# Performance work log

Hardware: AMD Instinct MI355X
Metric: run time of the kernel (lower is better)

Reference implementation:

```python
import jax, jax.numpy as jnp
import numpy as np

B, S, H = 2, 2048, 1024
NH, HD = 16, 64
WINDOW = 1024
ROPE_THETA = 10000.0
MAX_POS = 2048


def _rope_tables(dtype=jnp.float32):
    # RotaryEmbedding cache: inv_freq over even dims, emb = cat(freqs, freqs)
    inv_freq = 1.0 / (ROPE_THETA ** (jnp.arange(0, HD, 2, dtype=jnp.float32) / HD))
    t = jnp.arange(MAX_POS, dtype=jnp.float32)
    freqs = jnp.einsum('i,j->ij', t, inv_freq)          # [MAX_POS, HD//2]
    emb = jnp.concatenate([freqs, freqs], axis=-1)      # [MAX_POS, HD]
    return jnp.cos(emb).astype(dtype), jnp.sin(emb).astype(dtype)


def _rotate_half(x):
    x1, x2 = x[..., : HD // 2], x[..., HD // 2:]
    return jnp.concatenate([-x2, x1], axis=-1)


def setup_inputs() -> dict:
    key = jax.random.key(0)
    ks = jax.random.split(key, 5)
    sc = 0.02
    hidden_states = jax.random.normal(ks[0], (B, S, H), dtype=jnp.float32)
    position_ids = jnp.tile(jnp.arange(S, dtype=jnp.int64)[None, :], (B, 1))
    wq = jax.random.normal(ks[1], (H, H), dtype=jnp.float32) * sc
    wk = jax.random.normal(ks[2], (H, H), dtype=jnp.float32) * sc
    wv = jax.random.normal(ks[3], (H, H), dtype=jnp.float32) * sc
    wo = jax.random.normal(ks[4], (H, H), dtype=jnp.float32) * sc
    zeros = jnp.zeros((H,), dtype=jnp.float32)
    return {"hidden_states": hidden_states, "position_ids": position_ids,
            "wq": wq, "bq": zeros, "wk": wk, "bk": zeros,
            "wv": wv, "bv": zeros, "wo": wo, "bo": zeros}


def reference(hidden_states, position_ids, wq, bq, wk, bk, wv, bv, wo, bo):
    b, s, _ = hidden_states.shape
    # projections (nn.Linear: x @ W.T + b), split heads -> [B, NH, S, HD]
    def proj(w, bias):
        y = hidden_states @ w.T + bias
        return y.reshape(b, s, NH, HD).transpose(0, 2, 1, 3)
    q, k, v = proj(wq, bq), proj(wk, bk), proj(wv, bv)

    # RoPE: gather cos/sin at position_ids, broadcast over heads
    cos_t, sin_t = _rope_tables(hidden_states.dtype)
    pos = jnp.clip(position_ids, 0, MAX_POS - 1)
    cos = cos_t[pos][:, None, :, :]   # [B, 1, S, HD]
    sin = sin_t[pos][:, None, :, :]
    q = q * cos + _rotate_half(q) * sin
    k = k * cos + _rotate_half(k) * sin

    # scaled dot-product attention with causal + sliding-window band mask
    scores = jnp.einsum('bhqd,bhkd->bhqk', q, k) / jnp.sqrt(jnp.asarray(HD, hidden_states.dtype))
    i = jnp.arange(s)[:, None]
    j = jnp.arange(s)[None, :]
    allowed = (j <= i) & (i - j < WINDOW)          # banded causal mask [S, S]
    neg = jnp.asarray(jnp.finfo(hidden_states.dtype).min, hidden_states.dtype)
    scores = jnp.where(allowed[None, None, :, :], scores, neg)
    probs = jax.nn.softmax(scores, axis=-1)
    ctx = jnp.einsum('bhqk,bhkd->bhqd', probs, v)  # [B, NH, S, HD]
    ctx = ctx.transpose(0, 2, 1, 3).reshape(b, s, H)
    return ctx @ wo.T + bo
```

## Files before the change

### kernel.cpp

```cpp
#include <hip/hip_runtime.h>

#define BATCH 2
#define SDIM 2048
#define HDIM 1024
#define NHEADS 16
#define HEADD 64
#define WIN 1024

typedef __bf16 bf16x8 __attribute__((ext_vector_type(8)));
typedef __bf16 bf16x4 __attribute__((ext_vector_type(4)));
typedef float f32x4 __attribute__((ext_vector_type(4)));
typedef unsigned short u16x8 __attribute__((ext_vector_type(8)));

__device__ __forceinline__ unsigned short bf16_rne(float f) {
    union { float f; unsigned u; } x; x.f = f;
    unsigned r = x.u + 0x7fffu + ((x.u >> 16) & 1u);
    return (unsigned short)(r >> 16);
}

__device__ __forceinline__ void gload_lds16(const unsigned short* g, unsigned short* l) {
    __builtin_amdgcn_global_load_lds(
        (const __attribute__((address_space(1))) void*)g,
        (__attribute__((address_space(3))) void*)l, 16, 0, 0);
}

__global__ __launch_bounds__(256) void prep_kernel(
    const float* __restrict__ hs, const float* __restrict__ wq, const float* __restrict__ wk,
    const float* __restrict__ wv, const float* __restrict__ wo,
    unsigned short* __restrict__ Xb, unsigned short* __restrict__ Wqkv,
    unsigned short* __restrict__ Wob, float2* __restrict__ cstab)
{
    int i = blockIdx.x * 256 + threadIdx.x;
    if (i < 2097152) {
        const float* src; unsigned short* dst; int off;
        if (i < 1048576)      { src = hs; dst = Xb;             off = i; }
        else if (i < 1310720) { src = wq; dst = Wqkv;           off = i - 1048576; }
        else if (i < 1572864) { src = wk; dst = Wqkv + 1048576; off = i - 1310720; }
        else if (i < 1835008) { src = wv; dst = Wqkv + 2097152; off = i - 1572864; }
        else                  { src = wo; dst = Wob;            off = i - 1835008; }
        float4 v = reinterpret_cast<const float4*>(src)[off];
        ushort4 r;
        r.x = bf16_rne(v.x); r.y = bf16_rne(v.y); r.z = bf16_rne(v.z); r.w = bf16_rne(v.w);
        reinterpret_cast<ushort4*>(dst)[off] = r;
    } else {
        int j = i - 2097152;
        int p = j >> 5, f = j & 31;
        float inv = (float)pow(10000.0, -(double)f / 32.0);
        float ang = (float)p * inv;
        cstab[j] = make_float2(cosf(ang), sinf(ang));
    }
}

__global__ __launch_bounds__(256) void vtrans_kernel(
    const unsigned short* __restrict__ in, unsigned short* __restrict__ out)
{
    __shared__ __align__(16) unsigned short T[64 * 72];
    int s0 = blockIdx.x * 64, h = blockIdx.y, b = blockIdx.z;
    long hb = (long)(b * NHEADS + h) * SDIM * HEADD;
    int t = threadIdx.x;
    int sr = t >> 2, sc = (t & 3) * 16;
    u16x8 v0 = *(const u16x8*)&in[hb + (long)(s0 + sr) * HEADD + sc];
    u16x8 v1 = *(const u16x8*)&in[hb + (long)(s0 + sr) * HEADD + sc + 8];
    #pragma unroll
    for (int j = 0; j < 8; j++) {
        T[(sc + j) * 72     + (sr ^ (sc & 48))] = (unsigned short)v0[j];
        T[(sc + 8 + j) * 72 + (sr ^ (sc & 48))] = (unsigned short)v1[j];
    }
    __syncthreads();
    int dr = t >> 2, dc = (t & 3) * 16;
    int cb = dc ^ (dr & 48);
    u16x8 o0 = *(const u16x8*)&T[dr * 72 + cb];
    u16x8 o1 = *(const u16x8*)&T[dr * 72 + cb + 8];
    *(u16x8*)&out[hb + (long)dr * SDIM + s0 + dc]     = o0;
    *(u16x8*)&out[hb + (long)dr * SDIM + s0 + dc + 8] = o1;
}

__device__ __forceinline__ void mfma_gemm_128(
    const unsigned short* __restrict__ A,
    const unsigned short* __restrict__ Bm,
    int m0, int n0, int tid,
    unsigned short* lA, unsigned short* lB,
    f32x4 acc[4][4])
{
    const int K = 1024;
    const int BUF = 128 * 32;
    int lane = tid & 63, wid = tid >> 6;
    int wm = wid >> 1, wn = wid & 1;
    int lane15 = lane & 15, lhi = lane >> 4;
    int lrow = lane >> 2;
    int swz = (lane & 3) ^ ((lane >> 3) & 3);
    const unsigned short* ga0 = A  + (long)(m0 + wid * 32      + lrow) * K + swz * 8;
    const unsigned short* ga1 = A  + (long)(m0 + wid * 32 + 16 + lrow) * K + swz * 8;
    const unsigned short* gb0 = Bm + (long)(n0 + wid * 32      + lrow) * K + swz * 8;
    const unsigned short* gb1 = Bm + (long)(n0 + wid * 32 + 16 + lrow) * K + swz * 8;
    unsigned short* la0 = lA + (wid * 32)      * 32;
    unsigned short* la1 = lA + (wid * 32 + 16) * 32;
    unsigned short* lb0 = lB + (wid * 32)      * 32;
    unsigned short* lb1 = lB + (wid * 32 + 16) * 32;
    int ru = (lhi ^ ((lane15 >> 1) & 3)) * 8;

#define STAGE_G(boff, kt) \
    gload_lds16(ga0 + (kt) * 32, la0 + (boff)); \
    gload_lds16(ga1 + (kt) * 32, la1 + (boff)); \
    gload_lds16(gb0 + (kt) * 32, lb0 + (boff)); \
    gload_lds16(gb1 + (kt) * 32, lb1 + (boff));

#define COMPUTE_G(off) { \
    bf16x8 af[4], bfr[4]; \
    _Pragma("unroll") \
    for (int f = 0; f < 4; f++) { \
        af[f]  = *(const bf16x8*)&lA[(off) + (wm * 64 + f * 16 + lane15) * 32 + ru]; \
        bfr[f] = *(const bf16x8*)&lB[(off) + (wn * 64 + f * 16 + lane15) * 32 + ru]; \
    } \
    _Pragma("unroll") \
    for (int i = 0; i < 4; i++) \
        _Pragma("unroll") \
        for (int j = 0; j < 4; j++) \
            acc[i][j] = __builtin_amdgcn_mfma_f32_16x16x32_bf16(af[i], bfr[j], acc[i][j], 0, 0, 0); \
}

#define WAITB(n) \
    asm volatile("s_waitcnt vmcnt(" #n ")" ::: "memory"); \
    __builtin_amdgcn_s_barrier(); \
    asm volatile("" ::: "memory");

    STAGE_G(0, 0);
    STAGE_G(BUF, 1);
    #pragma unroll 1
    for (int t = 0; t < 30; t += 3) {
        WAITB(4);
        STAGE_G(2 * BUF, t + 2);
        COMPUTE_G(0);
        WAITB(4);
        STAGE_G(0, t + 3);
        COMPUTE_G(BUF);
        WAITB(4);
        STAGE_G(BUF, t + 4);
        COMPUTE_G(2 * BUF);
    }
    WAITB(4);
    COMPUTE_G(0);
    WAITB(0);
    COMPUTE_G(BUF);

#undef STAGE_G
#undef COMPUTE_G
#undef WAITB
}

__global__ __launch_bounds__(256) void gemm_qkv_kernel(
    const unsigned short* __restrict__ Xb,
    const unsigned short* __restrict__ Wb,
    const float* __restrict__ bq, const float* __restrict__ bk, const float* __restrict__ bv,
    const float2* __restrict__ cstab,
    unsigned short* __restrict__ qbuf, unsigned short* __restrict__ kbuf, unsigned short* __restrict__ vbuf)
{
    __shared__ __align__(16) unsigned short lA[3 * 128 * 32];
    __shared__ __align__(16) unsigned short lB[3 * 128 * 32];
    int tid = threadIdx.x;
    int lane = tid & 63, wid = tid >> 6;
    int wm = wid >> 1, wn = wid & 1;
    int lane15 = lane & 15, lhi = lane >> 4;
    int bid = blockIdx.x;
    int xcd = bid & 7, j5 = bid >> 3;
    int m0 = (xcd * 4 + (j5 & 3)) * 128;
    int n0 = (j5 >> 2) * 128;
    f32x4 acc[4][4];
    #pragma unroll
    for (int i = 0; i < 4; i++)
        #pragma unroll
        for (int j = 0; j < 4; j++)
            acc[i][j] = (f32x4){0.f, 0.f, 0.f, 0.f};

    mfma_gemm_128(Xb, Wb, m0, n0, tid, lA, lB, acc);

    int proj = n0 >> 10;
    int ncol0 = (n0 & 1023) + wn * 64;
    int h = ncol0 >> 6;
    unsigned short* dst = proj == 0 ? qbuf : (proj == 1 ? kbuf : vbuf);
    const float* bias = proj == 0 ? bq : (proj == 1 ? bk : bv);
    #pragma unroll
    for (int fm = 0; fm < 4; fm++) {
        #pragma unroll
        for (int reg = 0; reg < 4; reg++) {
            int m = m0 + wm * 64 + fm * 16 + lhi * 4 + reg;
            int bb = m >> 11, s = m & (SDIM - 1);
            long base = ((long)(bb * NHEADS + h) * SDIM + s) * HEADD;
            if (proj < 2) {
                #pragma unroll
                for (int fn = 0; fn < 2; fn++) {
                    int j = fn * 16 + lane15;
                    float lo = acc[fm][fn][reg]     + bias[ncol0 + j];
                    float hi = acc[fm][fn + 2][reg] + bias[ncol0 + 32 + j];
                    float2 cs = cstab[s * 32 + j];
                    float rl = lo * cs.x - hi * cs.y;
                    float rh = hi * cs.x + lo * cs.y;
                    if (proj == 0) { rl *= 0.125f; rh *= 0.125f; }
                    dst[base + j]      = bf16_rne(rl);
                    dst[base + 32 + j] = bf16_rne(rh);
                }
            } else {
                #pragma unroll
                for (int fn = 0; fn < 4; fn++) {
                    int d = fn * 16 + lane15;
                    dst[base + d] = bf16_rne(acc[fm][fn][reg] + bias[ncol0 + d]);
                }
            }
        }
    }
}

__global__ __launch_bounds__(512) void attn_kernel(
    const unsigned short* __restrict__ qb,
    const unsigned short* __restrict__ kbf,
    const unsigned short* __restrict__ vtb,
    unsigned short* __restrict__ ctxb)
{
    __shared__ __align__(16) unsigned short Kl[64 * 72];
    __shared__ __align__(16) unsigned short Vl[64 * 72];
    __shared__ __align__(16) unsigned short Pl[8][16 * 72];
    int tid = threadIdx.x, lane = tid & 63, wid = tid >> 6;
    int lane15 = lane & 15, lhi = lane >> 4;

    int slot = blockIdx.x;
    int xcd = slot & 7;
    int pos = slot >> 3;
    int hb32 = xcd + 8 * (pos >> 4);
    int h = hb32 & 15, b = hb32 >> 4;
    int qt = 15 - (pos & 15);
    int q0b = qt * 128;
    int qw = q0b + wid * 16;

    long hb = (long)(b * NHEADS + h) * SDIM * HEADD;
    const unsigned short* qptr = qb + hb;
    const unsigned short* kptr = kbf + hb;
    const unsigned short* vt   = vtb + hb;
    unsigned short* Pw = Pl[wid];

    bf16x8 aq0 = *(const bf16x8*)&qptr[(qw + lane15) * HEADD + lhi * 8];
    bf16x8 aq1 = *(const bf16x8*)&qptr[(qw + lane15) * HEADD + 32 + lhi * 8];

    f32x4 acc[4];
    #pragma unroll
    for (int f = 0; f < 4; f++) acc[f] = (f32x4){0.f, 0.f, 0.f, 0.f};
    float rs = 0.f;

    int t0 = q0b - (WIN - 1);
    int kb0 = t0 > 0 ? (t0 >> 6) : 0;
    int kbl = (q0b + 127) >> 6;
    int srow = tid >> 3;
    int sc = (tid & 7) * 8;

    u16x8 kr = *(const u16x8*)&kptr[(kb0 * 64 + srow) * HEADD + sc];
    u16x8 vr = *(const u16x8*)&vt[(long)srow * SDIM + kb0 * 64 + sc];

    for (int kblk = kb0; kblk <= kbl; kblk++) {
        int kbase = kblk * 64;
        __syncthreads();
        *(u16x8*)&Kl[srow * 72 + sc] = kr;
        *(u16x8*)&Vl[srow * 72 + sc] = vr;
        __syncthreads();
        if (kblk < kbl) {
            int nb = (kblk + 1) * 64;
            kr = *(const u16x8*)&kptr[(nb + srow) * HEADD + sc];
            vr = *(const u16x8*)&vt[(long)srow * SDIM + nb + sc];
        }
        if (kbase + 63 < qw - (WIN - 1)) continue;
        if (kbase > qw + 15) continue;

        bool full = (kbase + 63 <= qw) && (qw + 15 - kbase < WIN);
        f32x4 S[4];
        #pragma unroll
        for (int fk = 0; fk < 4; fk++) {
            bf16x8 bk0 = *(const bf16x8*)&Kl[(fk * 16 + lane15) * 72 + lhi * 8];
            bf16x8 bk1 = *(const bf16x8*)&Kl[(fk * 16 + lane15) * 72 + 32 + lhi * 8];
            f32x4 s = (f32x4){0.f, 0.f, 0.f, 0.f};
            s = __builtin_amdgcn_mfma_f32_16x16x32_bf16(bk0, aq0, s, 0, 0, 0);
            s = __builtin_amdgcn_mfma_f32_16x16x32_bf16(bk1, aq1, s, 0, 0, 0);
            S[fk] = s;
        }
        if (!full) {
            int q = qw + lane15;
            #pragma unroll
            for (int fk = 0; fk < 4; fk++)
                #pragma unroll
                for (int r = 0; r < 4; r++) {
                    int k = kbase + fk * 16 + lhi * 4 + r;
                    bool ok = (k <= q) && (q - k < WIN);
                    if (!ok) S[fk][r] = -1e30f;
                }
        }
        #pragma unroll
        for (int fk = 0; fk < 4; fk++) {
            bf16x4 c;
            #pragma unroll
            for (int r = 0; r < 4; r++) {
                float p = __expf(S[fk][r]);
                rs += p;
                c[r] = (__bf16)p;
            }
            *(bf16x4*)&Pw[lane15 * 72 + fk * 16 + lhi * 4] = c;
        }
        #pragma unroll
        for (int ks = 0; ks < 2; ks++) {
            bf16x8 pa = *(const bf16x8*)&Pw[lane15 * 72 + ks * 32 + lhi * 8];
            #pragma unroll
            for (int fd = 0; fd < 4; fd++) {
                bf16x8 bv2 = *(const bf16x8*)&Vl[(fd * 16 + lane15) * 72 + ks * 32 + lhi * 8];
                acc[fd] = __builtin_amdgcn_mfma_f32_16x16x32_bf16(pa, bv2, acc[fd], 0, 0, 0);
            }
        }
    }
    rs += __shfl_xor(rs, 16);
    rs += __shfl_xor(rs, 32);
    float linv[4];
    #pragma unroll
    for (int r = 0; r < 4; r++)
        linv[r] = 1.0f / __shfl(rs, lhi * 4 + r);
    #pragma unroll
    for (int fd = 0; fd < 4; fd++)
        #pragma unroll
        for (int r = 0; r < 4; r++) {
            int q = qw + lhi * 4 + r;
            int d = fd * 16 + lane15;
            ctxb[(((long)b * SDIM + q) * NHEADS + h) * HEADD + d] = bf16_rne(acc[fd][r] * linv[r]);
        }
}

__global__ __launch_bounds__(256) void gemm_o_kernel(
    const unsigned short* __restrict__ Ab,
    const unsigned short* __restrict__ Wb,
    const float* __restrict__ bo,
    float* __restrict__ out)
{
    __shared__ __align__(16) unsigned short lA[3 * 128 * 32];
    __shared__ __align__(16) unsigned short lB[3 * 128 * 32];
    int tid = threadIdx.x;
    int lane = tid & 63, wid = tid >> 6;
    int wm = wid >> 1, wn = wid & 1;
    int lane15 = lane & 15, lhi = lane >> 4;
    int bid = blockIdx.x;
    int xcd = bid & 7, j5 = bid >> 3;
    int m0 = (xcd * 4 + (j5 & 3)) * 128;
    int n0 = (j5 >> 2) * 128;
    f32x4 acc[4][4];
    #pragma unroll
    for (int i = 0; i < 4; i++)
        #pragma unroll
        for (int j = 0; j < 4; j++)
            acc[i][j] = (f32x4){0.f, 0.f, 0.f, 0.f};

    mfma_gemm_128(Ab, Wb, m0, n0, tid, lA, lB, acc);

    #pragma unroll
    for (int fm = 0; fm < 4; fm++)
        #pragma unroll
        for (int reg = 0; reg < 4; reg++) {
            int m = m0 + wm * 64 + fm * 16 + lhi * 4 + reg;
            #pragma unroll
            for (int fn = 0; fn < 4; fn++) {
                int n = n0 + wn * 64 + fn * 16 + lane15;
                out[(long)m * HDIM + n] = acc[fm][fn][reg] + bo[n];
            }
        }
}

extern "C" void kernel_launch(void* const* d_in, const int* in_sizes, int n_in,
                              void* d_out, int out_size, void* d_ws, size_t ws_size,
                              hipStream_t stream) {
    const float* hs = (const float*)d_in[0];
    const float* wq = (const float*)d_in[2];
    const float* bq = (const float*)d_in[3];
    const float* wk = (const float*)d_in[4];
    const float* bk = (const float*)d_in[5];
    const float* wv = (const float*)d_in[6];
    const float* bv = (const float*)d_in[7];
    const float* wo = (const float*)d_in[8];
    const float* bo = (const float*)d_in[9];
    float* out = (float*)d_out;

    char* ws = (char*)d_ws;
    unsigned short* Xb    = (unsigned short*)(ws);
    unsigned short* Wqkv  = (unsigned short*)(ws + (8l  << 20));
    unsigned short* Wob   = (unsigned short*)(ws + (14l << 20));
    float2*         cstab = (float2*)        (ws + (16l << 20));
    unsigned short* qbuf  = (unsigned short*)(ws + (17l << 20));
    unsigned short* kbuf  = (unsigned short*)(ws + (25l << 20));
    unsigned short* vbuf  = (unsigned short*)(ws + (33l << 20));
    unsigned short* ctxb  = (unsigned short*)(ws + (41l << 20));
    unsigned short* vT    = Xb;

    prep_kernel<<<8448, 256, 0, stream>>>(hs, wq, wk, wv, wo, Xb, Wqkv, Wob, cstab);
    gemm_qkv_kernel<<<768, 256, 0, stream>>>(Xb, Wqkv, bq, bk, bv, cstab, qbuf, kbuf, vbuf);
    vtrans_kernel<<<dim3(SDIM / 64, NHEADS, BATCH), 256, 0, stream>>>(vbuf, vT);
    attn_kernel<<<512, 512, 0, stream>>>(qbuf, kbuf, vT, ctxb);
    gemm_o_kernel<<<256, 256, 0, stream>>>(ctxb, Wob, bo, out);
}
```

Before: 111.1 us.

## Fuse V transpose into QKV GEMM epilogue via shared-memory staging

Removes the separate V-transpose kernel by having the QKV GEMM's V-projection blocks stage their output tile in shared memory and write V directly in [d][s] layout with vectorized stores. The GEMM main loop is inlined into the kernel and switched from a triple-buffered to a double-buffered LDS pipeline, so the same shared buffer can be reused for the transpose. This saves one launch plus a full read and write of V, at the cost of less prefetch depth in the GEMM and an extra LDS round-trip in the V epilogue.

Result: faster. 103.4 us (-6.9%).

```diff
diff --git a/kernel.cpp b/kernel.cpp
--- a/kernel.cpp
+++ b/kernel.cpp
@@ -51,30 +51,6 @@
     }
 }
 
-__global__ __launch_bounds__(256) void vtrans_kernel(
-    const unsigned short* __restrict__ in, unsigned short* __restrict__ out)
-{
-    __shared__ __align__(16) unsigned short T[64 * 72];
-    int s0 = blockIdx.x * 64, h = blockIdx.y, b = blockIdx.z;
-    long hb = (long)(b * NHEADS + h) * SDIM * HEADD;
-    int t = threadIdx.x;
-    int sr = t >> 2, sc = (t & 3) * 16;
-    u16x8 v0 = *(const u16x8*)&in[hb + (long)(s0 + sr) * HEADD + sc];
-    u16x8 v1 = *(const u16x8*)&in[hb + (long)(s0 + sr) * HEADD + sc + 8];
-    #pragma unroll
-    for (int j = 0; j < 8; j++) {
-        T[(sc + j) * 72     + (sr ^ (sc & 48))] = (unsigned short)v0[j];
-        T[(sc + 8 + j) * 72 + (sr ^ (sc & 48))] = (unsigned short)v1[j];
-    }
-    __syncthreads();
-    int dr = t >> 2, dc = (t & 3) * 16;
-    int cb = dc ^ (dr & 48);
-    u16x8 o0 = *(const u16x8*)&T[dr * 72 + cb];
-    u16x8 o1 = *(const u16x8*)&T[dr * 72 + cb + 8];
-    *(u16x8*)&out[hb + (long)dr * SDIM + s0 + dc]     = o0;
-    *(u16x8*)&out[hb + (long)dr * SDIM + s0 + dc + 8] = o1;
-}
-
 __device__ __forceinline__ void mfma_gemm_128(
     const unsigned short* __restrict__ A,
     const unsigned short* __restrict__ Bm,
@@ -155,8 +131,11 @@
     const float2* __restrict__ cstab,
     unsigned short* __restrict__ qbuf, unsigned short* __restrict__ kbuf, unsigned short* __restrict__ vbuf)
 {
-    __shared__ __align__(16) unsigned short lA[3 * 128 * 32];
-    __shared__ __align__(16) unsigned short lB[3 * 128 * 32];
+    const int K = 1024;
+    const int BUF = 128 * 32;
+    __shared__ __align__(16) unsigned short smem[4 * 128 * 32];
+    unsigned short* lA = smem;
+    unsigned short* lB = smem + 2 * BUF;
     int tid = threadIdx.x;
     int lane = tid & 63, wid = tid >> 6;
     int wm = wid >> 1, wn = wid & 1;
@@ -165,6 +144,18 @@
     int xcd = bid & 7, j5 = bid >> 3;
     int m0 = (xcd * 4 + (j5 & 3)) * 128;
     int n0 = (j5 >> 2) * 128;
+    int lrow = lane >> 2;
+    int swz = (lane & 3) ^ ((lane >> 3) & 3);
+    const unsigned short* ga0 = Xb + (long)(m0 + wid * 32      + lrow) * K + swz * 8;
+    const unsigned short* ga1 = Xb + (long)(m0 + wid * 32 + 16 + lrow) * K + swz * 8;
+    const unsigned short* gb0 = Wb + (long)(n0 + wid * 32      + lrow) * K + swz * 8;
+    const unsigned short* gb1 = Wb + (long)(n0 + wid * 32 + 16 + lrow) * K + swz * 8;
+    unsigned short* la0 = lA + (wid * 32)      * 32;
+    unsigned short* la1 = lA + (wid * 32 + 16) * 32;
+    unsigned short* lb0 = lB + (wid * 32)      * 32;
+    unsigned short* lb1 = lB + (wid * 32 + 16) * 32;
+    int ru = (lhi ^ ((lane15 >> 1) & 3)) * 8;
+
     f32x4 acc[4][4];
     #pragma unroll
     for (int i = 0; i < 4; i++)
@@ -172,21 +163,92 @@
         for (int j = 0; j < 4; j++)
             acc[i][j] = (f32x4){0.f, 0.f, 0.f, 0.f};
 
-    mfma_gemm_128(Xb, Wb, m0, n0, tid, lA, lB, acc);
+#define STAGE_Q(boff, kt) \
+    gload_lds16(ga0 + (kt) * 32, la0 + (boff)); \
+    gload_lds16(ga1 + (kt) * 32, la1 + (boff)); \
+    gload_lds16(gb0 + (kt) * 32, lb0 + (boff)); \
+    gload_lds16(gb1 + (kt) * 32, lb1 + (boff));
+
+#define COMPUTE_Q(off) { \
+    bf16x8 af[4], bfr[4]; \
+    _Pragma("unroll") \
+    for (int f = 0; f < 4; f++) { \
+        af[f]  = *(const bf16x8*)&lA[(off) + (wm * 64 + f * 16 + lane15) * 32 + ru]; \
+        bfr[f] = *(const bf16x8*)&lB[(off) + (wn * 64 + f * 16 + lane15) * 32 + ru]; \
+    } \
+    _Pragma("unroll") \
+    for (int i = 0; i < 4; i++) \
+        _Pragma("unroll") \
+        for (int j = 0; j < 4; j++) \
+            acc[i][j] = __builtin_amdgcn_mfma_f32_16x16x32_bf16(af[i], bfr[j], acc[i][j], 0, 0, 0); \
+}
+
+#define WAITQ(n) \
+    asm volatile("s_waitcnt vmcnt(" #n ")" ::: "memory"); \
+    __builtin_amdgcn_s_barrier(); \
+    asm volatile("" ::: "memory");
+
+    STAGE_Q(0, 0);
+    STAGE_Q(BUF, 1);
+    #pragma unroll 1
+    for (int t = 0; t < 30; t += 2) {
+        WAITQ(4);
+        COMPUTE_Q(0);
+        __builtin_amdgcn_s_barrier();
+        STAGE_Q(0, t + 2);
+        WAITQ(4);
+        COMPUTE_Q(BUF);
+        __builtin_amdgcn_s_barrier();
+        STAGE_Q(BUF, t + 3);
+    }
+    WAITQ(4);
+    COMPUTE_Q(0);
+    WAITQ(0);
+    COMPUTE_Q(BUF);
+
+#undef STAGE_Q
+#undef COMPUTE_Q
+#undef WAITQ
 
     int proj = n0 >> 10;
     int ncol0 = (n0 & 1023) + wn * 64;
     int h = ncol0 >> 6;
-    unsigned short* dst = proj == 0 ? qbuf : (proj == 1 ? kbuf : vbuf);
-    const float* bias = proj == 0 ? bq : (proj == 1 ? bk : bv);
-    #pragma unroll
-    for (int fm = 0; fm < 4; fm++) {
-        #pragma unroll
-        for (int reg = 0; reg < 4; reg++) {
-            int m = m0 + wm * 64 + fm * 16 + lhi * 4 + reg;
-            int bb = m >> 11, s = m & (SDIM - 1);
-            long base = ((long)(bb * NHEADS + h) * SDIM + s) * HEADD;
-            if (proj < 2) {
+    int bb = m0 >> 11, s0r = m0 & (SDIM - 1);
+    if (proj == 2) {
+        const float* bias = bv;
+        __syncthreads();
+        #pragma unroll
+        for (int fm = 0; fm < 4; fm++)
+            #pragma unroll
+            for (int reg = 0; reg < 4; reg++) {
+                int sl = wm * 64 + fm * 16 + lhi * 4 + reg;
+                #pragma unroll
+                for (int fn = 0; fn < 4; fn++) {
+                    int dl = wn * 64 + fn * 16 + lane15;
+                    float v = acc[fm][fn][reg] + bias[(n0 & 1023) + dl];
+                    smem[dl * 128 + (sl ^ ((dl & 7) * 8))] = bf16_rne(v);
+                }
+            }
+        __syncthreads();
+        int h0 = (n0 & 1023) >> 6;
+        #pragma unroll
+        for (int it = 0; it < 8; it++) {
+            int d = it * 16 + (tid >> 4);
+            int s8 = tid & 15;
+            u16x8 valv = *(const u16x8*)&smem[d * 128 + ((s8 ^ (d & 7)) * 8)];
+            int hh = h0 + (d >> 6);
+            *(u16x8*)&vbuf[((long)(bb * NHEADS + hh) * HEADD + (d & 63)) * SDIM + s0r + s8 * 8] = valv;
+        }
+    } else {
+        unsigned short* dst = proj == 0 ? qbuf : kbuf;
+        const float* bias = proj == 0 ? bq : bk;
+        #pragma unroll
+        for (int fm = 0; fm < 4; fm++) {
+            #pragma unroll
+            for (int reg = 0; reg < 4; reg++) {
+                int m = m0 + wm * 64 + fm * 16 + lhi * 4 + reg;
+                int s = m & (SDIM - 1);
+                long base = ((long)(bb * NHEADS + h) * SDIM + s) * HEADD;
                 #pragma unroll
                 for (int fn = 0; fn < 2; fn++) {
                     int j = fn * 16 + lane15;
@@ -198,12 +260,6 @@
                     if (proj == 0) { rl *= 0.125f; rh *= 0.125f; }
                     dst[base + j]      = bf16_rne(rl);
                     dst[base + 32 + j] = bf16_rne(rh);
-                }
-            } else {
-                #pragma unroll
-                for (int fn = 0; fn < 4; fn++) {
-                    int d = fn * 16 + lane15;
-                    dst[base + d] = bf16_rne(acc[fm][fn][reg] + bias[ncol0 + d]);
                 }
             }
         }
@@ -388,11 +444,9 @@
     unsigned short* kbuf  = (unsigned short*)(ws + (25l << 20));
     unsigned short* vbuf  = (unsigned short*)(ws + (33l << 20));
     unsigned short* ctxb  = (unsigned short*)(ws + (41l << 20));
-    unsigned short* vT    = Xb;
 
     prep_kernel<<<8448, 256, 0, stream>>>(hs, wq, wk, wv, wo, Xb, Wqkv, Wob, cstab);
     gemm_qkv_kernel<<<768, 256, 0, stream>>>(Xb, Wqkv, bq, bk, bv, cstab, qbuf, kbuf, vbuf);
-    vtrans_kernel<<<dim3(SDIM / 64, NHEADS, BATCH), 256, 0, stream>>>(vbuf, vT);
-    attn_kernel<<<512, 512, 0, stream>>>(qbuf, kbuf, vT, ctxb);
+    attn_kernel<<<512, 512, 0, stream>>>(qbuf, kbuf, vbuf, ctxb);
     gemm_o_kernel<<<256, 256, 0, stream>>>(ctxb, Wob, bo, out);
 }
```

## Fuse V transpose into QKV GEMM epilogue and double-buffer attention K/V loads

Applied to the files above, without the earlier changes.

The QKV GEMM epilogue now stages the V tile in LDS with an XOR swizzle and writes V directly in transposed [head, d, s] layout. This removes the separate transpose kernel and its global round trip. The attention kernel replaces its register-staged K/V loads with direct global-to-LDS loads into a double buffer, prefetching two blocks ahead and using an XOR swizzle instead of padding. This should overlap memory with compute and save a launch, but it adds extra barriers in the GEMM epilogue and relies on careful vmcnt accounting.

Measured after the change: 113.4 us. 1.02x slower.

```diff
diff --git a/kernel.cpp b/kernel.cpp
--- a/kernel.cpp
+++ b/kernel.cpp
@@ -51,30 +51,6 @@
     }
 }
 
-__global__ __launch_bounds__(256) void vtrans_kernel(
-    const unsigned short* __restrict__ in, unsigned short* __restrict__ out)
-{
-    __shared__ __align__(16) unsigned short T[64 * 72];
-    int s0 = blockIdx.x * 64, h = blockIdx.y, b = blockIdx.z;
-    long hb = (long)(b * NHEADS + h) * SDIM * HEADD;
-    int t = threadIdx.x;
-    int sr = t >> 2, sc = (t & 3) * 16;
-    u16x8 v0 = *(const u16x8*)&in[hb + (long)(s0 + sr) * HEADD + sc];
-    u16x8 v1 = *(const u16x8*)&in[hb + (long)(s0 + sr) * HEADD + sc + 8];
-    #pragma unroll
-    for (int j = 0; j < 8; j++) {
-        T[(sc + j) * 72     + (sr ^ (sc & 48))] = (unsigned short)v0[j];
-        T[(sc + 8 + j) * 72 + (sr ^ (sc & 48))] = (unsigned short)v1[j];
-    }
-    __syncthreads();
-    int dr = t >> 2, dc = (t & 3) * 16;
-    int cb = dc ^ (dr & 48);
-    u16x8 o0 = *(const u16x8*)&T[dr * 72 + cb];
-    u16x8 o1 = *(const u16x8*)&T[dr * 72 + cb + 8];
-    *(u16x8*)&out[hb + (long)dr * SDIM + s0 + dc]     = o0;
-    *(u16x8*)&out[hb + (long)dr * SDIM + s0 + dc + 8] = o1;
-}
-
 __device__ __forceinline__ void mfma_gemm_128(
     const unsigned short* __restrict__ A,
     const unsigned short* __restrict__ Bm,
@@ -177,16 +153,44 @@
     int proj = n0 >> 10;
     int ncol0 = (n0 & 1023) + wn * 64;
     int h = ncol0 >> 6;
-    unsigned short* dst = proj == 0 ? qbuf : (proj == 1 ? kbuf : vbuf);
-    const float* bias = proj == 0 ? bq : (proj == 1 ? bk : bv);
-    #pragma unroll
-    for (int fm = 0; fm < 4; fm++) {
-        #pragma unroll
-        for (int reg = 0; reg < 4; reg++) {
-            int m = m0 + wm * 64 + fm * 16 + lhi * 4 + reg;
-            int bb = m >> 11, s = m & (SDIM - 1);
-            long base = ((long)(bb * NHEADS + h) * SDIM + s) * HEADD;
-            if (proj < 2) {
+    int bb = m0 >> 11, s0r = m0 & (SDIM - 1);
+    if (proj == 2) {
+        const float* bias = bv;
+        __syncthreads();
+        #pragma unroll
+        for (int fm = 0; fm < 4; fm++) {
+            int sl0 = wm * 64 + fm * 16 + lhi * 4;
+            #pragma unroll
+            for (int fn = 0; fn < 4; fn++) {
+                int dl = wn * 64 + fn * 16 + lane15;
+                float bia = bias[(n0 & 1023) + dl];
+                bf16x4 c;
+                #pragma unroll
+                for (int reg = 0; reg < 4; reg++)
+                    c[reg] = (__bf16)(acc[fm][fn][reg] + bia);
+                *(bf16x4*)&lA[dl * 128 + (sl0 ^ ((dl & 7) * 8))] = c;
+            }
+        }
+        __syncthreads();
+        int h0 = (n0 & 1023) >> 6;
+        #pragma unroll
+        for (int it = 0; it < 8; it++) {
+            int d = it * 16 + (tid >> 4);
+            int s8 = tid & 15;
+            u16x8 valv = *(const u16x8*)&lA[d * 128 + ((s8 ^ (d & 7)) * 8)];
+            int hh = h0 + (d >> 6);
+            *(u16x8*)&vbuf[((long)(bb * NHEADS + hh) * HEADD + (d & 63)) * SDIM + s0r + s8 * 8] = valv;
+        }
+    } else {
+        unsigned short* dst = proj == 0 ? qbuf : kbuf;
+        const float* bias = proj == 0 ? bq : bk;
+        #pragma unroll
+        for (int fm = 0; fm < 4; fm++) {
+            #pragma unroll
+            for (int reg = 0; reg < 4; reg++) {
+                int m = m0 + wm * 64 + fm * 16 + lhi * 4 + reg;
+                int s = m & (SDIM - 1);
+                long base = ((long)(bb * NHEADS + h) * SDIM + s) * HEADD;
                 #pragma unroll
                 for (int fn = 0; fn < 2; fn++) {
                     int j = fn * 16 + lane15;
@@ -199,12 +203,6 @@
                     dst[base + j]      = bf16_rne(rl);
                     dst[base + 32 + j] = bf16_rne(rh);
                 }
-            } else {
-                #pragma unroll
-                for (int fn = 0; fn < 4; fn++) {
-                    int d = fn * 16 + lane15;
-                    dst[base + d] = bf16_rne(acc[fm][fn][reg] + bias[ncol0 + d]);
-                }
             }
         }
     }
@@ -216,8 +214,9 @@
     const unsigned short* __restrict__ vtb,
     unsigned short* __restrict__ ctxb)
 {
-    __shared__ __align__(16) unsigned short Kl[64 * 72];
-    __shared__ __align__(16) unsigned short Vl[64 * 72];
+    const int TBUF = 64 * 64;
+    __shared__ __align__(16) unsigned short Kl[2 * TBUF];
+    __shared__ __align__(16) unsigned short Vl[2 * TBUF];
     __shared__ __align__(16) unsigned short Pl[8][16 * 72];
     int tid = threadIdx.x, lane = tid & 63, wid = tid >> 6;
     int lane15 = lane & 15, lhi = lane >> 4;
@@ -248,68 +247,82 @@
     int t0 = q0b - (WIN - 1);
     int kb0 = t0 > 0 ? (t0 >> 6) : 0;
     int kbl = (q0b + 127) >> 6;
-    int srow = tid >> 3;
-    int sc = (tid & 7) * 8;
-
-    u16x8 kr = *(const u16x8*)&kptr[(kb0 * 64 + srow) * HEADD + sc];
-    u16x8 vr = *(const u16x8*)&vt[(long)srow * SDIM + kb0 * 64 + sc];
-
+
+    int srow = (wid * 8) + ((lane >> 3) & 7);
+    int p8 = lane & 7;
+    int u8 = p8 ^ (srow & 7);
+    const unsigned short* kg = kptr + (long)srow * HEADD + u8 * 8;
+    const unsigned short* vg = vt + (long)srow * SDIM + u8 * 8;
+    unsigned short* lK = Kl + srow * 64 + p8 * 8;
+    unsigned short* lV = Vl + srow * 64 + p8 * 8;
+
+    gload_lds16(kg + (long)kb0 * 64 * HEADD, lK);
+    gload_lds16(vg + kb0 * 64, lV);
+    gload_lds16(kg + (long)(kb0 + 1) * 64 * HEADD, lK + TBUF);
+    gload_lds16(vg + (kb0 + 1) * 64, lV + TBUF);
+
+    int cur = 0;
     for (int kblk = kb0; kblk <= kbl; kblk++) {
+        if (kblk < kbl) { asm volatile("s_waitcnt vmcnt(2)" ::: "memory"); }
+        else            { asm volatile("s_waitcnt vmcnt(0)" ::: "memory"); }
+        __syncthreads();
         int kbase = kblk * 64;
-        __syncthreads();
-        *(u16x8*)&Kl[srow * 72 + sc] = kr;
-        *(u16x8*)&Vl[srow * 72 + sc] = vr;
-        __syncthreads();
-        if (kblk < kbl) {
-            int nb = (kblk + 1) * 64;
-            kr = *(const u16x8*)&kptr[(nb + srow) * HEADD + sc];
-            vr = *(const u16x8*)&vt[(long)srow * SDIM + nb + sc];
-        }
-        if (kbase + 63 < qw - (WIN - 1)) continue;
-        if (kbase > qw + 15) continue;
-
-        bool full = (kbase + 63 <= qw) && (qw + 15 - kbase < WIN);
-        f32x4 S[4];
-        #pragma unroll
-        for (int fk = 0; fk < 4; fk++) {
-            bf16x8 bk0 = *(const bf16x8*)&Kl[(fk * 16 + lane15) * 72 + lhi * 8];
-            bf16x8 bk1 = *(const bf16x8*)&Kl[(fk * 16 + lane15) * 72 + 32 + lhi * 8];
-            f32x4 s = (f32x4){0.f, 0.f, 0.f, 0.f};
-            s = __builtin_amdgcn_mfma_f32_16x16x32_bf16(bk0, aq0, s, 0, 0, 0);
-            s = __builtin_amdgcn_mfma_f32_16x16x32_bf16(bk1, aq1, s, 0, 0, 0);
-            S[fk] = s;
-        }
-        if (!full) {
-            int q = qw + lane15;
-            #pragma unroll
-            for (int fk = 0; fk < 4; fk++)
+        bool active = !(kbase + 63 < qw - (WIN - 1)) && !(kbase > qw + 15);
+        if (active) {
+            const unsigned short* Kc = Kl + cur * TBUF;
+            const unsigned short* Vc = Vl + cur * TBUF;
+            bool full = (kbase + 63 <= qw) && (qw + 15 - kbase < WIN);
+            f32x4 S[4];
+            #pragma unroll
+            for (int fk = 0; fk < 4; fk++) {
+                int row = fk * 16 + lane15;
+                int r7 = (row & 7);
+                bf16x8 bk0 = *(const bf16x8*)&Kc[row * 64 + ((lhi ^ r7) * 8)];
+                bf16x8 bk1 = *(const bf16x8*)&Kc[row * 64 + (((4 + lhi) ^ r7) * 8)];
+                f32x4 s = (f32x4){0.f, 0.f, 0.f, 0.f};
+                s = __builtin_amdgcn_mfma_f32_16x16x32_bf16(bk0, aq0, s, 0, 0, 0);
+                s = __builtin_amdgcn_mfma_f32_16x16x32_bf16(bk1, aq1, s, 0, 0, 0);
+                S[fk] = s;
+            }
+            if (!full) {
+                int q = qw + lane15;
+                #pragma unroll
+                for (int fk = 0; fk < 4; fk++)
+                    #pragma unroll
+                    for (int r = 0; r < 4; r++) {
+                        int k = kbase + fk * 16 + lhi * 4 + r;
+                        bool ok = (k <= q) && (q - k < WIN);
+                        if (!ok) S[fk][r] = -1e30f;
+                    }
+            }
+            #pragma unroll
+            for (int fk = 0; fk < 4; fk++) {
+                bf16x4 c;
                 #pragma unroll
                 for (int r = 0; r < 4; r++) {
-                    int k = kbase + fk * 16 + lhi * 4 + r;
-                    bool ok = (k <= q) && (q - k < WIN);
-                    if (!ok) S[fk][r] = -1e30f;
+                    float pv = __expf(S[fk][r]);
+                    rs += pv;
+                    c[r] = (__bf16)pv;
                 }
-        }
-        #pragma unroll
-        for (int fk = 0; fk < 4; fk++) {
-            bf16x4 c;
-            #pragma unroll
-            for (int r = 0; r < 4; r++) {
-                float p = __expf(S[fk][r]);
-                rs += p;
-                c[r] = (__bf16)p;
-            }
-            *(bf16x4*)&Pw[lane15 * 72 + fk * 16 + lhi * 4] = c;
-        }
-        #pragma unroll
-        for (int ks = 0; ks < 2; ks++) {
-            bf16x8 pa = *(const bf16x8*)&Pw[lane15 * 72 + ks * 32 + lhi * 8];
-            #pragma unroll
-            for (int fd = 0; fd < 4; fd++) {
-                bf16x8 bv2 = *(const bf16x8*)&Vl[(fd * 16 + lane15) * 72 + ks * 32 + lhi * 8];
-                acc[fd] = __builtin_amdgcn_mfma_f32_16x16x32_bf16(pa, bv2, acc[fd], 0, 0, 0);
-            }
-        }
+                *(bf16x4*)&Pw[lane15 * 72 + fk * 16 + lhi * 4] = c;
+            }
+            #pragma unroll
+            for (int ks = 0; ks < 2; ks++) {
+                bf16x8 pa = *(const bf16x8*)&Pw[lane15 * 72 + ks * 32 + lhi * 8];
+                #pragma unroll
+                for (int fd = 0; fd < 4; fd++) {
+                    int row = fd * 16 + lane15;
+                    bf16x8 bv2 = *(const bf16x8*)&Vc[row * 64 + (((ks * 4 + lhi) ^ (row & 7)) * 8)];
+                    acc[fd] = __builtin_amdgcn_mfma_f32_16x16x32_bf16(pa, bv2, acc[fd], 0, 0, 0);
+                }
+            }
+        }
+        __syncthreads();
+        if (kblk + 2 <= kbl) {
+            gload_lds16(kg + (long)(kblk + 2) * 64 * HEADD, lK + cur * TBUF);
+            gload_lds16(vg + (kblk + 2) * 64, lV + cur * TBUF);
+        }
+        cur ^= 1;
     }
     rs += __shfl_xor(rs, 16);
     rs += __shfl_xor(rs, 32);
@@ -388,11 +401,9 @@
     unsigned short* kbuf  = (unsigned short*)(ws + (25l << 20));
     unsigned short* vbuf  = (unsigned short*)(ws + (33l << 20));
     unsigned short* ctxb  = (unsigned short*)(ws + (41l << 20));
-    unsigned short* vT    = Xb;
 
     prep_kernel<<<8448, 256, 0, stream>>>(hs, wq, wk, wv, wo, Xb, Wqkv, Wob, cstab);
     gemm_qkv_kernel<<<768, 256, 0, stream>>>(Xb, Wqkv, bq, bk, bv, cstab, qbuf, kbuf, vbuf);
-    vtrans_kernel<<<dim3(SDIM / 64, NHEADS, BATCH), 256, 0, stream>>>(vbuf, vT);
-    attn_kernel<<<512, 512, 0, stream>>>(qbuf, kbuf, vT, ctxb);
+    attn_kernel<<<512, 512, 0, stream>>>(qbuf, kbuf, vbuf, ctxb);
     gemm_o_kernel<<<256, 256, 0, stream>>>(ctxb, Wob, bo, out);
 }
```
